# Kernel optimization log

Hardware: AMD Instinct MI355X
Metric: run time of the kernel (lower is better)

Reference implementation:

```python
import jax, jax.numpy as jnp
import numpy as np

N_NODES = 50000
N_EDGES = 800000
DIM = 100

def setup_inputs() -> dict:
    key = jax.random.key(0)
    k1, k2, k3, k4, k5, k6 = jax.random.split(key, 6)
    ego_embedding = jax.random.normal(k1, (N_NODES, DIM), dtype=jnp.float32)
    edge_src = jax.random.randint(k2, (N_EDGES,), 0, N_NODES, dtype=jnp.int32)
    edge_dst = jax.random.randint(k3, (N_EDGES,), 0, N_NODES, dtype=jnp.int32)
    edge_weight = jax.random.uniform(k4, (N_EDGES,), dtype=jnp.float32)
    W = jax.random.normal(k5, (DIM, DIM), dtype=jnp.float32) * (1.0 / np.sqrt(DIM))
    b = jax.random.normal(k6, (DIM,), dtype=jnp.float32) * 0.01
    return {"ego_embedding": ego_embedding, "edge_src": edge_src,
            "edge_dst": edge_dst, "edge_weight": edge_weight, "W": W, "b": b}

def reference(ego_embedding, edge_src, edge_dst, edge_weight, W, b):
    # Linear projection: h = x @ W^T + b  (torch Linear convention)
    hidden = ego_embedding @ W.T + b                    # [N, D]
    # u_mul_e: message on each edge = h[src] * edge_weight
    msgs = hidden[edge_src] * edge_weight[:, None]       # [E, D]
    # sum reduce into destination nodes
    out = jax.ops.segment_sum(msgs, edge_dst, num_segments=N_NODES)  # [N, D]
    return out
```

## Files before the change

### kernel.cpp

```cpp
#include <hip/hip_runtime.h>

#define N_NODES 50000
#define N_EDGES 800000
#define DIM 100

#define SB_COUNT 98
#define CAP1     8704
#define NB       1563
#define CAPB     768
#define OVF_CAP  4096
#define EPB1     2048
#define BIN1_BLOCKS 391
#define GEMM_BLOCKS 1250
#define ROWS_PB  40
#define SPLIT2   8

#define HIDB_OFF  0u
#define G1_OFF    10000448u
#define OVFC_OFF  10000960u
#define CNT2_OFF  10001024u
#define OVF_OFF   10007296u
#define BKT1_OFF  10072832u
#define BKT2_OFF  16896768u
#define WT_OFF    26530560u
#define WS_NEED   26570560u

__device__ inline unsigned bf16hi(float v) {
    unsigned u = __float_as_uint(v);
    u += 0x7FFFu + ((u >> 16) & 1u);
    return u & 0xFFFF0000u;
}
__device__ inline unsigned bf16pair(float lo, float hi) {
    unsigned ulo = __float_as_uint(lo); ulo += 0x7FFFu + ((ulo >> 16) & 1u);
    unsigned uhi = __float_as_uint(hi); uhi += 0x7FFFu + ((uhi >> 16) & 1u);
    return (ulo >> 16) | (uhi & 0xFFFF0000u);
}

__global__ __launch_bounds__(256) void srgnn_transpose(
    const float* __restrict__ W, float* __restrict__ Wt,
    int* __restrict__ gcur1, int* __restrict__ cnt2, int* __restrict__ ovfc)
{
    const unsigned i = blockIdx.x * 256u + threadIdx.x;
    if (i < DIM * DIM) {
        const int c = i / DIM, k = i - c * DIM;
        Wt[k * DIM + c] = W[i];
    }
    if (i < SB_COUNT) gcur1[i] = 0;
    if (i < SB_COUNT * 16) cnt2[i] = 0;
    if (i == 0) *ovfc = 0;
}

__global__ __launch_bounds__(256) void srgnn_gemm_bin1(
    const float* __restrict__ x, const float* __restrict__ Wt,
    const float* __restrict__ b, unsigned* __restrict__ hidU,
    const int* __restrict__ esrc, const int* __restrict__ edst,
    const float* __restrict__ ew, int* __restrict__ gcur1,
    int* __restrict__ ovfc, int4* __restrict__ ovf, uint2* __restrict__ bkt1)
{
    __shared__ float xs[ROWS_PB][DIM];
    __shared__ int hist[SB_COUNT];
    __shared__ int lcur[SB_COUNT];
    const int t = threadIdx.x;

    if (blockIdx.x < GEMM_BLOCKS) {
        const int row0 = blockIdx.x * ROWS_PB;

        for (int i = t; i < ROWS_PB * 25; i += 256) {
            const int r = i / 25, c4 = (i - r * 25) * 4;
            const float4 v = *reinterpret_cast<const float4*>(
                &x[(size_t)(row0 + r) * DIM + c4]);
            *reinterpret_cast<float4*>(&xs[r][c4]) = v;
        }
        __syncthreads();

        if (t < 250) {
            const int g  = t / 25;
            const int c4 = (t - g * 25) * 4;
            const float4 bv = *reinterpret_cast<const float4*>(&b[c4]);
            float4 a0 = bv, a1 = bv, a2 = bv, a3 = bv;

            #pragma unroll 4
            for (int k = 0; k < DIM; ++k) {
                const float4 wv = *reinterpret_cast<const float4*>(&Wt[k * DIM + c4]);
                const float x0 = xs[g     ][k];
                const float x1 = xs[g + 10][k];
                const float x2 = xs[g + 20][k];
                const float x3 = xs[g + 30][k];
                a0.x += x0 * wv.x; a0.y += x0 * wv.y; a0.z += x0 * wv.z; a0.w += x0 * wv.w;
                a1.x += x1 * wv.x; a1.y += x1 * wv.y; a1.z += x1 * wv.z; a1.w += x1 * wv.w;
                a2.x += x2 * wv.x; a2.y += x2 * wv.y; a2.z += x2 * wv.z; a2.w += x2 * wv.w;
                a3.x += x3 * wv.x; a3.y += x3 * wv.y; a3.z += x3 * wv.z; a3.w += x3 * wv.w;
            }
            const int u0 = c4 >> 1;
            uint2 p;
            p.x = bf16pair(a0.x, a0.y); p.y = bf16pair(a0.z, a0.w);
            *reinterpret_cast<uint2*>(&hidU[(size_t)(row0 + g     ) * 50 + u0]) = p;
            p.x = bf16pair(a1.x, a1.y); p.y = bf16pair(a1.z, a1.w);
            *reinterpret_cast<uint2*>(&hidU[(size_t)(row0 + g + 10) * 50 + u0]) = p;
            p.x = bf16pair(a2.x, a2.y); p.y = bf16pair(a2.z, a2.w);
            *reinterpret_cast<uint2*>(&hidU[(size_t)(row0 + g + 20) * 50 + u0]) = p;
            p.x = bf16pair(a3.x, a3.y); p.y = bf16pair(a3.z, a3.w);
            *reinterpret_cast<uint2*>(&hidU[(size_t)(row0 + g + 30) * 50 + u0]) = p;
        }
    } else {
        const int kb = blockIdx.x - GEMM_BLOCKS;
        const int e0 = kb * EPB1;

        for (int i = t; i < SB_COUNT; i += 256) hist[i] = 0;
        __syncthreads();

        int d[8];
        #pragma unroll
        for (int k = 0; k < 8; ++k) {
            const int e = e0 + t + k * 256;
            d[k] = (e < N_EDGES) ? edst[e] : -1;
            if (d[k] >= 0) atomicAdd(&hist[d[k] >> 9], 1);
        }
        __syncthreads();
        for (int i = t; i < SB_COUNT; i += 256)
            if (hist[i]) lcur[i] = atomicAdd(&gcur1[i], hist[i]);
        __syncthreads();
        #pragma unroll
        for (int k = 0; k < 8; ++k) {
            if (d[k] >= 0) {
                const int e = e0 + t + k * 256;
                const int s = esrc[e];
                const float w = ew[e];
                const int sb = d[k] >> 9;
                const int pos = atomicAdd(&lcur[sb], 1);
                if (pos < CAP1) {
                    bkt1[(size_t)sb * CAP1 + pos] =
                        make_uint2((unsigned)s | bf16hi(w), (unsigned)d[k]);
                } else {
                    const int op = atomicAdd(ovfc, 1);
                    if (op < OVF_CAP) ovf[op] = make_int4(d[k], s, __float_as_int(w), 0);
                }
            }
        }
    }
}

__global__ __launch_bounds__(256) void srgnn_bin2(
    const int* __restrict__ gcur1, const uint2* __restrict__ bkt1,
    int* __restrict__ cnt2, int* __restrict__ ovfc, int4* __restrict__ ovf,
    uint2* __restrict__ bkt2)
{
    __shared__ int histr[8][16];
    __shared__ int cur[16];
    const int t = threadIdx.x;
    const int sb = blockIdx.x >> 3;
    const int chunk = blockIdx.x & 7;
    const int rep = t & 7;

    int cnt = gcur1[sb];
    if (cnt > CAP1) cnt = CAP1;
    const int clen = (cnt + SPLIT2 - 1) >> 3;
    const int i0 = chunk * clen;
    int i1 = i0 + clen;
    if (i1 > cnt) i1 = cnt;

    if (t < 128) histr[t >> 4][t & 15] = 0;
    __syncthreads();

    for (int i = i0 + t; i < i1; i += 256) {
        const uint2 r = bkt1[(size_t)sb * CAP1 + i];
        atomicAdd(&histr[rep][(r.y >> 5) & 15], 1);
    }
    __syncthreads();

    if (t < 16) {
        int tot = 0;
        #pragma unroll
        for (int r = 0; r < 8; ++r) tot += histr[r][t];
        cur[t] = tot ? atomicAdd(&cnt2[sb * 16 + t], tot) : 0;
    }
    __syncthreads();

    for (int i = i0 + t; i < i1; i += 256) {
        const uint2 r = bkt1[(size_t)sb * CAP1 + i];
        const int j = (r.y >> 5) & 15;
        const int pos = atomicAdd(&cur[j], 1);
        if (pos < CAPB) {
            bkt2[(size_t)(sb * 16 + j) * CAPB + pos] = r;
        } else {
            const int op = atomicAdd(ovfc, 1);
            if (op < OVF_CAP)
                ovf[op] = make_int4((int)r.y, (int)(r.x & 0xFFFFu),
                                    (int)(r.x & 0xFFFF0000u), 0);
        }
    }
}

__global__ __launch_bounds__(256) void srgnn_agg_s32(
    const unsigned* __restrict__ hidU, const int* __restrict__ cnt2,
    const uint2* __restrict__ bkt2, const int* __restrict__ ovfc,
    const int4* __restrict__ ovf, float* __restrict__ out)
{
    __shared__ uint2    recs[CAPB];
    __shared__ unsigned srt[CAPB];
    __shared__ int nh[32], sc[32], cur[32];

    const int t = threadIdx.x;
    const int bq = blockIdx.x;
    int cntb = cnt2[bq];
    if (cntb > CAPB) cntb = CAPB;

    if (t < 32) nh[t] = 0;
    __syncthreads();
    for (int i = t; i < cntb; i += 256) {
        const uint2 r = bkt2[(size_t)bq * CAPB + i];
        recs[i] = r;
        atomicAdd(&nh[r.y & 31], 1);
    }
    __syncthreads();
    if (t < 32) sc[t] = nh[t];
    __syncthreads();
    for (int ofs = 1; ofs < 32; ofs <<= 1) {
        int a = 0;
        if (t < 32 && t >= ofs) a = sc[t - ofs];
        __syncthreads();
        if (t < 32) sc[t] += a;
        __syncthreads();
    }
    if (t < 32) cur[t] = sc[t] - nh[t];
    __syncthreads();
    for (int i = t; i < cntb; i += 256) {
        const uint2 r = recs[i];
        const int pos = atomicAdd(&cur[r.y & 31], 1);
        srt[pos] = r.x;
    }
    __syncthreads();

    int oc = *ovfc;
    if (oc > OVF_CAP) oc = OVF_CAP;
    const int lane = t & 63;
    const int wid  = t >> 6;
    const bool active = (lane < 50);

    for (int q = 0; q < 8; ++q) {
        const int n  = wid * 8 + q;
        const int s1 = sc[n];
        const int s0 = s1 - nh[n];
        float2 acc = make_float2(0.f, 0.f);

        int p = s0;
        for (; p + 8 <= s1; p += 8) {
            unsigned r[8], h[8];
            #pragma unroll
            for (int j = 0; j < 8; ++j) r[j] = srt[p + j];
            if (active) {
                #pragma unroll
                for (int j = 0; j < 8; ++j)
                    h[j] = hidU[(size_t)(r[j] & 0xFFFFu) * 50 + lane];
                #pragma unroll
                for (int j = 0; j < 8; ++j) {
                    const float wj = __uint_as_float(r[j] & 0xFFFF0000u);
                    acc.x += wj * __uint_as_float(h[j] << 16);
                    acc.y += wj * __uint_as_float(h[j] & 0xFFFF0000u);
                }
            }
        }
        for (; p < s1; ++p) {
            const unsigned r = srt[p];
            const float wi = __uint_as_float(r & 0xFFFF0000u);
            if (active) {
                const unsigned h = hidU[(size_t)(r & 0xFFFFu) * 50 + lane];
                acc.x += wi * __uint_as_float(h << 16);
                acc.y += wi * __uint_as_float(h & 0xFFFF0000u);
            }
        }

        const int ng = bq * 32 + n;
        if (oc > 0) {
            for (int i = 0; i < oc; ++i) {
                const int4 v = ovf[i];
                if (v.x == ng && active) {
                    const unsigned h = hidU[(size_t)v.y * 50 + lane];
                    const float wi = __uint_as_float((unsigned)v.z);
                    acc.x += wi * __uint_as_float(h << 16);
                    acc.y += wi * __uint_as_float(h & 0xFFFF0000u);
                }
            }
        }
        if (ng < N_NODES && active)
            *reinterpret_cast<float2*>(&out[(size_t)ng * DIM + 2 * lane]) = acc;
    }
}

__global__ __launch_bounds__(256) void srgnn_gemm_bias(
    const float* __restrict__ x, const float* __restrict__ W,
    const float* __restrict__ b, float* __restrict__ hidden)
{
    __shared__ float Wt[DIM][DIM + 4];
    __shared__ float bs[DIM];
    __shared__ float xs[8][DIM];
    const int t = threadIdx.x;
    for (int i = t; i < DIM * DIM; i += 256) {
        int c = i / DIM, k = i - c * DIM;
        Wt[k][c] = W[i];
    }
    if (t < DIM) bs[t] = b[t];
    const int row0 = blockIdx.x * 8;
    for (int i = t; i < 8 * DIM; i += 256) {
        int r = i / DIM, k = i - r * DIM;
        int row = row0 + r;
        xs[r][k] = (row < N_NODES) ? x[row * DIM + k] : 0.0f;
    }
    __syncthreads();
    if (t < 200) {
        const int r  = t / 25;
        const int c4 = (t - r * 25) * 4;
        float acc0 = bs[c4 + 0], acc1 = bs[c4 + 1], acc2 = bs[c4 + 2], acc3 = bs[c4 + 3];
        for (int k = 0; k < DIM; ++k) {
            const float xv = xs[r][k];
            const float4 wv = *reinterpret_cast<const float4*>(&Wt[k][c4]);
            acc0 += xv * wv.x; acc1 += xv * wv.y; acc2 += xv * wv.z; acc3 += xv * wv.w;
        }
        const int row = row0 + r;
        if (row < N_NODES)
            *reinterpret_cast<float4*>(&hidden[row * DIM + c4]) =
                make_float4(acc0, acc1, acc2, acc3);
    }
}

__global__ __launch_bounds__(256) void srgnn_scatter_atomic(
    const float* __restrict__ hidden, const int* __restrict__ esrc,
    const int* __restrict__ edst, const float* __restrict__ ew,
    float* __restrict__ out)
{
    const unsigned gid = blockIdx.x * 256u + threadIdx.x;
    const unsigned e = gid / 25u;
    const unsigned j = gid - e * 25u;
    if (e >= N_EDGES) return;
    const int   s  = esrc[e];
    const int   d  = edst[e];
    const float wt = ew[e];
    const float4 h = *reinterpret_cast<const float4*>(&hidden[(size_t)s * DIM + j * 4]);
    float* op = &out[(size_t)d * DIM + j * 4];
    atomicAdd(op + 0, h.x * wt);
    atomicAdd(op + 1, h.y * wt);
    atomicAdd(op + 2, h.z * wt);
    atomicAdd(op + 3, h.w * wt);
}

extern "C" void kernel_launch(void* const* d_in, const int* in_sizes, int n_in,
                              void* d_out, int out_size, void* d_ws, size_t ws_size,
                              hipStream_t stream) {
    const float* x    = (const float*)d_in[0];
    const int*   esrc = (const int*)  d_in[1];
    const int*   edst = (const int*)  d_in[2];
    const float* ew   = (const float*)d_in[3];
    const float* W    = (const float*)d_in[4];
    const float* b    = (const float*)d_in[5];
    float* out = (float*)d_out;

    char* ws = (char*)d_ws;

    if (ws_size >= WS_NEED) {
        unsigned* hidU  = (unsigned*)(ws + HIDB_OFF);
        int*      gcur1 = (int*)     (ws + G1_OFF);
        int*      ovfc  = (int*)     (ws + OVFC_OFF);
        int*      cnt2  = (int*)     (ws + CNT2_OFF);
        int4*     ovf   = (int4*)    (ws + OVF_OFF);
        uint2*    bkt1  = (uint2*)   (ws + BKT1_OFF);
        uint2*    bkt2  = (uint2*)   (ws + BKT2_OFF);
        float*    Wt    = (float*)   (ws + WT_OFF);

        srgnn_transpose<<<(DIM * DIM + 255) / 256, 256, 0, stream>>>(
            W, Wt, gcur1, cnt2, ovfc);
        srgnn_gemm_bin1<<<GEMM_BLOCKS + BIN1_BLOCKS, 256, 0, stream>>>(
            x, Wt, b, hidU, esrc, edst, ew, gcur1, ovfc, ovf, bkt1);
        srgnn_bin2<<<SB_COUNT * SPLIT2, 256, 0, stream>>>(
            gcur1, bkt1, cnt2, ovfc, ovf, bkt2);
        srgnn_agg_s32<<<NB, 256, 0, stream>>>(hidU, cnt2, bkt2, ovfc, ovf, out);
    } else {
        float* hidden = (float*)ws;
        hipMemsetAsync(d_out, 0, (size_t)out_size * sizeof(float), stream);
        const int gemm_blocks = (N_NODES + 7) / 8;
        srgnn_gemm_bias<<<gemm_blocks, 256, 0, stream>>>(x, W, b, hidden);
        const long long work = (long long)N_EDGES * 25;
        const int scat_blocks = (int)((work + 255) / 256);
        srgnn_scatter_atomic<<<scat_blocks, 256, 0, stream>>>(hidden, esrc, edst, ew, out);
    }
}
```

Measured before the change: 80.50 us.

## Drop second binning pass; aggregate 64-node chunks directly from superbucket records

Removes the bin2 pass and its intermediate bucket array. Each aggregation block now scans its entire 512-node superbucket of records (about 8K) and keeps only the records for its 64-node chunk, then sorts them in shared memory before aggregating. The GEMM is split back into its own kernel, which stages W^T in shared memory, and binning runs as a separate launch. In exchange, every superbucket's records are read 8 times by the aggregation blocks, and the GEMM and binning no longer overlap within one launch.

```diff
diff --git a/kernel.cpp b/kernel.cpp
--- a/kernel.cpp
+++ b/kernel.cpp
@@ -6,24 +6,21 @@
 
 #define SB_COUNT 98
 #define CAP1     8704
-#define NB       1563
-#define CAPB     768
 #define OVF_CAP  4096
 #define EPB1     2048
 #define BIN1_BLOCKS 391
 #define GEMM_BLOCKS 1250
 #define ROWS_PB  40
-#define SPLIT2   8
+#define SPLITA   8
+#define SRT_CAP  2048
 
 #define HIDB_OFF  0u
-#define G1_OFF    10000448u
-#define OVFC_OFF  10000960u
-#define CNT2_OFF  10001024u
-#define OVF_OFF   10007296u
-#define BKT1_OFF  10072832u
-#define BKT2_OFF  16896768u
-#define WT_OFF    26530560u
-#define WS_NEED   26570560u
+#define G1_OFF    10000000u
+#define OVFC_OFF  10000448u
+#define OVF_OFF   10000464u
+#define BKT1_OFF  10066048u
+#define WT_OFF    16889984u
+#define WS_NEED   16929984u
 
 __device__ inline unsigned bf16hi(float v) {
     unsigned u = __float_as_uint(v);
@@ -38,7 +35,7 @@
 
 __global__ __launch_bounds__(256) void srgnn_transpose(
     const float* __restrict__ W, float* __restrict__ Wt,
-    int* __restrict__ gcur1, int* __restrict__ cnt2, int* __restrict__ ovfc)
+    int* __restrict__ gcur1, int* __restrict__ ovfc)
 {
     const unsigned i = blockIdx.x * 256u + threadIdx.x;
     if (i < DIM * DIM) {
@@ -46,188 +43,146 @@
         Wt[k * DIM + c] = W[i];
     }
     if (i < SB_COUNT) gcur1[i] = 0;
-    if (i < SB_COUNT * 16) cnt2[i] = 0;
     if (i == 0) *ovfc = 0;
 }
 
-__global__ __launch_bounds__(256) void srgnn_gemm_bin1(
-    const float* __restrict__ x, const float* __restrict__ Wt,
-    const float* __restrict__ b, unsigned* __restrict__ hidU,
+__global__ __launch_bounds__(256, 2) void srgnn_gemm3(
+    const float* __restrict__ x, const float* __restrict__ Wtg,
+    const float* __restrict__ b, unsigned* __restrict__ hidU)
+{
+    __shared__ float Wt[DIM][DIM];
+    __shared__ float xs[ROWS_PB][DIM];
+    const int t = threadIdx.x;
+    const int row0 = blockIdx.x * ROWS_PB;
+
+    for (int i = t; i < 2500; i += 256) {
+        const float4 v = *reinterpret_cast<const float4*>(&Wtg[i * 4]);
+        *reinterpret_cast<float4*>(&Wt[0][0] + i * 4) = v;
+    }
+    for (int i = t; i < ROWS_PB * 25; i += 256) {
+        const int r = i / 25, c4 = (i - r * 25) * 4;
+        const float4 v = *reinterpret_cast<const float4*>(
+            &x[(size_t)(row0 + r) * DIM + c4]);
+        *reinterpret_cast<float4*>(&xs[r][c4]) = v;
+    }
+    __syncthreads();
+
+    if (t < 250) {
+        const int g  = t / 25;
+        const int c4 = (t - g * 25) * 4;
+        const float4 bv = *reinterpret_cast<const float4*>(&b[c4]);
+        float4 a0 = bv, a1 = bv, a2 = bv, a3 = bv;
+
+        #pragma unroll 4
+        for (int k = 0; k < DIM; ++k) {
+            const float4 wv = *reinterpret_cast<const float4*>(&Wt[k][c4]);
+            const float x0 = xs[g     ][k];
+            const float x1 = xs[g + 10][k];
+            const float x2 = xs[g + 20][k];
+            const float x3 = xs[g + 30][k];
+            a0.x += x0 * wv.x; a0.y += x0 * wv.y; a0.z += x0 * wv.z; a0.w += x0 * wv.w;
+            a1.x += x1 * wv.x; a1.y += x1 * wv.y; a1.z += x1 * wv.z; a1.w += x1 * wv.w;
+            a2.x += x2 * wv.x; a2.y += x2 * wv.y; a2.z += x2 * wv.z; a2.w += x2 * wv.w;
+            a3.x += x3 * wv.x; a3.y += x3 * wv.y; a3.z += x3 * wv.z; a3.w += x3 * wv.w;
+        }
+        const int u0 = c4 >> 1;
+        uint2 p;
+        p.x = bf16pair(a0.x, a0.y); p.y = bf16pair(a0.z, a0.w);
+        *reinterpret_cast<uint2*>(&hidU[(size_t)(row0 + g     ) * 50 + u0]) = p;
+        p.x = bf16pair(a1.x, a1.y); p.y = bf16pair(a1.z, a1.w);
+        *reinterpret_cast<uint2*>(&hidU[(size_t)(row0 + g + 10) * 50 + u0]) = p;
+        p.x = bf16pair(a2.x, a2.y); p.y = bf16pair(a2.z, a2.w);
+        *reinterpret_cast<uint2*>(&hidU[(size_t)(row0 + g + 20) * 50 + u0]) = p;
+        p.x = bf16pair(a3.x, a3.y); p.y = bf16pair(a3.z, a3.w);
+        *reinterpret_cast<uint2*>(&hidU[(size_t)(row0 + g + 30) * 50 + u0]) = p;
+    }
+}
+
+__global__ __launch_bounds__(256) void srgnn_bin1(
     const int* __restrict__ esrc, const int* __restrict__ edst,
     const float* __restrict__ ew, int* __restrict__ gcur1,
     int* __restrict__ ovfc, int4* __restrict__ ovf, uint2* __restrict__ bkt1)
 {
-    __shared__ float xs[ROWS_PB][DIM];
     __shared__ int hist[SB_COUNT];
     __shared__ int lcur[SB_COUNT];
     const int t = threadIdx.x;
-
-    if (blockIdx.x < GEMM_BLOCKS) {
-        const int row0 = blockIdx.x * ROWS_PB;
-
-        for (int i = t; i < ROWS_PB * 25; i += 256) {
-            const int r = i / 25, c4 = (i - r * 25) * 4;
-            const float4 v = *reinterpret_cast<const float4*>(
-                &x[(size_t)(row0 + r) * DIM + c4]);
-            *reinterpret_cast<float4*>(&xs[r][c4]) = v;
-        }
-        __syncthreads();
-
-        if (t < 250) {
-            const int g  = t / 25;
-            const int c4 = (t - g * 25) * 4;
-            const float4 bv = *reinterpret_cast<const float4*>(&b[c4]);
-            float4 a0 = bv, a1 = bv, a2 = bv, a3 = bv;
-
-            #pragma unroll 4
-            for (int k = 0; k < DIM; ++k) {
-                const float4 wv = *reinterpret_cast<const float4*>(&Wt[k * DIM + c4]);
-                const float x0 = xs[g     ][k];
-                const float x1 = xs[g + 10][k];
-                const float x2 = xs[g + 20][k];
-                const float x3 = xs[g + 30][k];
-                a0.x += x0 * wv.x; a0.y += x0 * wv.y; a0.z += x0 * wv.z; a0.w += x0 * wv.w;
-                a1.x += x1 * wv.x; a1.y += x1 * wv.y; a1.z += x1 * wv.z; a1.w += x1 * wv.w;
-                a2.x += x2 * wv.x; a2.y += x2 * wv.y; a2.z += x2 * wv.z; a2.w += x2 * wv.w;
-                a3.x += x3 * wv.x; a3.y += x3 * wv.y; a3.z += x3 * wv.z; a3.w += x3 * wv.w;
+    const int e0 = blockIdx.x * EPB1;
+
+    for (int i = t; i < SB_COUNT; i += 256) hist[i] = 0;
+    __syncthreads();
+
+    int d[8];
+    #pragma unroll
+    for (int k = 0; k < 8; ++k) {
+        const int e = e0 + t + k * 256;
+        d[k] = (e < N_EDGES) ? edst[e] : -1;
+        if (d[k] >= 0) atomicAdd(&hist[d[k] >> 9], 1);
+    }
+    __syncthreads();
+    for (int i = t; i < SB_COUNT; i += 256)
+        if (hist[i]) lcur[i] = atomicAdd(&gcur1[i], hist[i]);
+    __syncthreads();
+    #pragma unroll
+    for (int k = 0; k < 8; ++k) {
+        if (d[k] >= 0) {
+            const int e = e0 + t + k * 256;
+            const int s = esrc[e];
+            const float w = ew[e];
+            const int sb = d[k] >> 9;
+            const int pos = atomicAdd(&lcur[sb], 1);
+            if (pos < CAP1) {
+                bkt1[(size_t)sb * CAP1 + pos] =
+                    make_uint2((unsigned)s | bf16hi(w), (unsigned)d[k]);
+            } else {
+                const int op = atomicAdd(ovfc, 1);
+                if (op < OVF_CAP) ovf[op] = make_int4(d[k], s, __float_as_int(w), 0);
             }
-            const int u0 = c4 >> 1;
-            uint2 p;
-            p.x = bf16pair(a0.x, a0.y); p.y = bf16pair(a0.z, a0.w);
-            *reinterpret_cast<uint2*>(&hidU[(size_t)(row0 + g     ) * 50 + u0]) = p;
-            p.x = bf16pair(a1.x, a1.y); p.y = bf16pair(a1.z, a1.w);
-            *reinterpret_cast<uint2*>(&hidU[(size_t)(row0 + g + 10) * 50 + u0]) = p;
-            p.x = bf16pair(a2.x, a2.y); p.y = bf16pair(a2.z, a2.w);
-            *reinterpret_cast<uint2*>(&hidU[(size_t)(row0 + g + 20) * 50 + u0]) = p;
-            p.x = bf16pair(a3.x, a3.y); p.y = bf16pair(a3.z, a3.w);
-            *reinterpret_cast<uint2*>(&hidU[(size_t)(row0 + g + 30) * 50 + u0]) = p;
-        }
-    } else {
-        const int kb = blockIdx.x - GEMM_BLOCKS;
-        const int e0 = kb * EPB1;
-
-        for (int i = t; i < SB_COUNT; i += 256) hist[i] = 0;
-        __syncthreads();
-
-        int d[8];
-        #pragma unroll
-        for (int k = 0; k < 8; ++k) {
-            const int e = e0 + t + k * 256;
-            d[k] = (e < N_EDGES) ? edst[e] : -1;
-            if (d[k] >= 0) atomicAdd(&hist[d[k] >> 9], 1);
-        }
-        __syncthreads();
-        for (int i = t; i < SB_COUNT; i += 256)
-            if (hist[i]) lcur[i] = atomicAdd(&gcur1[i], hist[i]);
-        __syncthreads();
-        #pragma unroll
-        for (int k = 0; k < 8; ++k) {
-            if (d[k] >= 0) {
-                const int e = e0 + t + k * 256;
-                const int s = esrc[e];
-                const float w = ew[e];
-                const int sb = d[k] >> 9;
-                const int pos = atomicAdd(&lcur[sb], 1);
-                if (pos < CAP1) {
-                    bkt1[(size_t)sb * CAP1 + pos] =
-                        make_uint2((unsigned)s | bf16hi(w), (unsigned)d[k]);
-                } else {
-                    const int op = atomicAdd(ovfc, 1);
-                    if (op < OVF_CAP) ovf[op] = make_int4(d[k], s, __float_as_int(w), 0);
-                }
-            }
-        }
-    }
-}
-
-__global__ __launch_bounds__(256) void srgnn_bin2(
-    const int* __restrict__ gcur1, const uint2* __restrict__ bkt1,
-    int* __restrict__ cnt2, int* __restrict__ ovfc, int4* __restrict__ ovf,
-    uint2* __restrict__ bkt2)
-{
-    __shared__ int histr[8][16];
-    __shared__ int cur[16];
+        }
+    }
+}
+
+__global__ __launch_bounds__(256) void srgnn_agg_sb(
+    const unsigned* __restrict__ hidU, const int* __restrict__ gcur1,
+    const uint2* __restrict__ bkt1, const int* __restrict__ ovfc,
+    const int4* __restrict__ ovf, float* __restrict__ out)
+{
+    __shared__ unsigned srt[SRT_CAP];
+    __shared__ int nh[64], sc[64], cur[64];
+
     const int t = threadIdx.x;
     const int sb = blockIdx.x >> 3;
     const int chunk = blockIdx.x & 7;
-    const int rep = t & 7;
+    const unsigned key = (unsigned)chunk;
 
     int cnt = gcur1[sb];
     if (cnt > CAP1) cnt = CAP1;
-    const int clen = (cnt + SPLIT2 - 1) >> 3;
-    const int i0 = chunk * clen;
-    int i1 = i0 + clen;
-    if (i1 > cnt) i1 = cnt;
-
-    if (t < 128) histr[t >> 4][t & 15] = 0;
-    __syncthreads();
-
-    for (int i = i0 + t; i < i1; i += 256) {
+
+    if (t < 64) nh[t] = 0;
+    __syncthreads();
+
+    for (int i = t; i < cnt; i += 256) {
         const uint2 r = bkt1[(size_t)sb * CAP1 + i];
-        atomicAdd(&histr[rep][(r.y >> 5) & 15], 1);
-    }
-    __syncthreads();
-
-    if (t < 16) {
-        int tot = 0;
-        #pragma unroll
-        for (int r = 0; r < 8; ++r) tot += histr[r][t];
-        cur[t] = tot ? atomicAdd(&cnt2[sb * 16 + t], tot) : 0;
-    }
-    __syncthreads();
-
-    for (int i = i0 + t; i < i1; i += 256) {
+        if (((r.y >> 6) & 7u) == key) atomicAdd(&nh[r.y & 63], 1);
+    }
+    __syncthreads();
+    if (t < 64) sc[t] = nh[t];
+    __syncthreads();
+    for (int ofs = 1; ofs < 64; ofs <<= 1) {
+        int a = 0;
+        if (t < 64 && t >= ofs) a = sc[t - ofs];
+        __syncthreads();
+        if (t < 64) sc[t] += a;
+        __syncthreads();
+    }
+    if (t < 64) cur[t] = sc[t] - nh[t];
+    __syncthreads();
+
+    for (int i = t; i < cnt; i += 256) {
         const uint2 r = bkt1[(size_t)sb * CAP1 + i];
-        const int j = (r.y >> 5) & 15;
-        const int pos = atomicAdd(&cur[j], 1);
-        if (pos < CAPB) {
-            bkt2[(size_t)(sb * 16 + j) * CAPB + pos] = r;
-        } else {
-            const int op = atomicAdd(ovfc, 1);
-            if (op < OVF_CAP)
-                ovf[op] = make_int4((int)r.y, (int)(r.x & 0xFFFFu),
-                                    (int)(r.x & 0xFFFF0000u), 0);
-        }
-    }
-}
-
-__global__ __launch_bounds__(256) void srgnn_agg_s32(
-    const unsigned* __restrict__ hidU, const int* __restrict__ cnt2,
-    const uint2* __restrict__ bkt2, const int* __restrict__ ovfc,
-    const int4* __restrict__ ovf, float* __restrict__ out)
-{
-    __shared__ uint2    recs[CAPB];
-    __shared__ unsigned srt[CAPB];
-    __shared__ int nh[32], sc[32], cur[32];
-
-    const int t = threadIdx.x;
-    const int bq = blockIdx.x;
-    int cntb = cnt2[bq];
-    if (cntb > CAPB) cntb = CAPB;
-
-    if (t < 32) nh[t] = 0;
-    __syncthreads();
-    for (int i = t; i < cntb; i += 256) {
-        const uint2 r = bkt2[(size_t)bq * CAPB + i];
-        recs[i] = r;
-        atomicAdd(&nh[r.y & 31], 1);
-    }
-    __syncthreads();
-    if (t < 32) sc[t] = nh[t];
-    __syncthreads();
-    for (int ofs = 1; ofs < 32; ofs <<= 1) {
-        int a = 0;
-        if (t < 32 && t >= ofs) a = sc[t - ofs];
-        __syncthreads();
-        if (t < 32) sc[t] += a;
-        __syncthreads();
-    }
-    if (t < 32) cur[t] = sc[t] - nh[t];
-    __syncthreads();
-    for (int i = t; i < cntb; i += 256) {
-        const uint2 r = recs[i];
-        const int pos = atomicAdd(&cur[r.y & 31], 1);
-        srt[pos] = r.x;
+        if (((r.y >> 6) & 7u) == key) {
+            const int pos = atomicAdd(&cur[r.y & 63], 1);
+            if (pos < SRT_CAP) srt[pos] = r.x;
+        }
     }
     __syncthreads();
 
@@ -237,8 +192,8 @@
     const int wid  = t >> 6;
     const bool active = (lane < 50);
 
-    for (int q = 0; q < 8; ++q) {
-        const int n  = wid * 8 + q;
+    for (int q = 0; q < 16; ++q) {
+        const int n  = wid * 16 + q;
         const int s1 = sc[n];
         const int s0 = s1 - nh[n];
         float2 acc = make_float2(0.f, 0.f);
@@ -270,13 +225,13 @@
             }
         }
 
-        const int ng = bq * 32 + n;
+        const int ng = sb * 512 + chunk * 64 + n;
         if (oc > 0) {
             for (int i = 0; i < oc; ++i) {
                 const int4 v = ovf[i];
                 if (v.x == ng && active) {
                     const unsigned h = hidU[(size_t)v.y * 50 + lane];
-                    const float wi = __uint_as_float((unsigned)v.z);
+                    const float wi = __int_as_float(v.z);
                     acc.x += wi * __uint_as_float(h << 16);
                     acc.y += wi * __uint_as_float(h & 0xFFFF0000u);
                 }
@@ -360,19 +315,17 @@
         unsigned* hidU  = (unsigned*)(ws + HIDB_OFF);
         int*      gcur1 = (int*)     (ws + G1_OFF);
         int*      ovfc  = (int*)     (ws + OVFC_OFF);
-        int*      cnt2  = (int*)     (ws + CNT2_OFF);
         int4*     ovf   = (int4*)    (ws + OVF_OFF);
         uint2*    bkt1  = (uint2*)   (ws + BKT1_OFF);
-        uint2*    bkt2  = (uint2*)   (ws + BKT2_OFF);
         float*    Wt    = (float*)   (ws + WT_OFF);
 
         srgnn_transpose<<<(DIM * DIM + 255) / 256, 256, 0, stream>>>(
-            W, Wt, gcur1, cnt2, ovfc);
-        srgnn_gemm_bin1<<<GEMM_BLOCKS + BIN1_BLOCKS, 256, 0, stream>>>(
-            x, Wt, b, hidU, esrc, edst, ew, gcur1, ovfc, ovf, bkt1);
-        srgnn_bin2<<<SB_COUNT * SPLIT2, 256, 0, stream>>>(
-            gcur1, bkt1, cnt2, ovfc, ovf, bkt2);
-        srgnn_agg_s32<<<NB, 256, 0, stream>>>(hidU, cnt2, bkt2, ovfc, ovf, out);
+            W, Wt, gcur1, ovfc);
+        srgnn_gemm3<<<GEMM_BLOCKS, 256, 0, stream>>>(x, Wt, b, hidU);
+        srgnn_bin1<<<BIN1_BLOCKS, 256, 0, stream>>>(
+            esrc, edst, ew, gcur1, ovfc, ovf, bkt1);
+        srgnn_agg_sb<<<SB_COUNT * SPLITA, 256, 0, stream>>>(
+            hidU, gcur1, bkt1, ovfc, ovf, out);
     } else {
         float* hidden = (float*)ws;
         hipMemsetAsync(d_out, 0, (size_t)out_size * sizeof(float), stream);
```

Measured after the change: 124.8 us. +55.0%, slower.
